# Performance work log

Hardware: AMD Instinct MI355X
Metric: run time of the kernel (lower is better)

The kernel has to match this reference:

```python
import jax, jax.numpy as jnp
import numpy as np

B, N = 2, 131072          # batch, expanded node slots (divisible by flag_size)
FEAT = 69                 # org(3) + pos(3) + uids(63)
KERNELS = 128
FLAG_SIZE = 4             # 1 << dims, dims = 2
BINS = 16                 # 1 << flag_size


def _conv1d(x, w, b, stride=1, padding='SAME'):
    # keras Conv1D: x [B,N,Cin], w [K,Cin,Cout], relu activation
    y = jax.lax.conv_general_dilated(x, w, (stride,), padding,
                                     dimension_numbers=('NWC', 'WIO', 'NWC'))
    return jax.nn.relu(y + b)


def setup_inputs() -> dict:
    key = jax.random.key(0)
    ks = jax.random.split(key, 12)

    def g(k, shape):
        fan_in = int(np.prod(shape[:-1]))
        return (jax.random.normal(k, shape, jnp.float32) / np.sqrt(fan_in)).astype(jnp.float32)

    c_x = FEAT + KERNELS                 # 197 after each pre conv concat
    c_flags = 2 * FEAT + KERNELS         # 266 flags-head input
    c_sym = c_flags + FLAG_SIZE          # 270 symbols-branch input

    return {
        'inputs': jax.random.normal(ks[0], (B, N, FEAT), jnp.float32),
        'w_pre0': g(ks[1], (3, FEAT, KERNELS)),   'b_pre0': jnp.zeros((KERNELS,), jnp.float32),
        'w_pre1': g(ks[2], (3, c_x, KERNELS)),    'b_pre1': jnp.zeros((KERNELS,), jnp.float32),
        'w_flags': g(ks[3], (c_flags, FLAG_SIZE)), 'b_flags': jnp.zeros((FLAG_SIZE,), jnp.float32),
        'w_merge': g(ks[4], (FLAG_SIZE, c_sym, KERNELS)), 'b_merge': jnp.zeros((KERNELS,), jnp.float32),
        'w_post0': g(ks[5], (3, KERNELS, KERNELS)), 'b_post0': jnp.zeros((KERNELS,), jnp.float32),
        'w_post1': g(ks[6], (3, KERNELS, KERNELS)), 'b_post1': jnp.zeros((KERNELS,), jnp.float32),
        'w_post2': g(ks[7], (3, KERNELS, KERNELS)), 'b_post2': jnp.zeros((KERNELS,), jnp.float32),
        'w_post3': g(ks[8], (3, KERNELS, KERNELS)), 'b_post3': jnp.zeros((KERNELS,), jnp.float32),
        'w_sym': g(ks[9], (KERNELS, BINS)),        'b_sym': jnp.zeros((BINS,), jnp.float32),
    }


def _forward(inputs, w_pre0, b_pre0, w_pre1, b_pre1, w_flags, b_flags,
             w_merge, b_merge, w_post0, b_post0, w_post1, b_post1,
             w_post2, b_post2, w_post3, b_post3, w_sym, b_sym):
    # pos offsets = (3, 6); pos = inputs[..., 3:5] (2 columns)
    pos = inputs[..., 3:5]
    sort = jnp.argsort(pos, axis=-2)                       # [B, N, 2]
    # gather with batch_dims=1 along node axis
    X = jnp.take_along_axis(inputs, sort[..., 1:2], axis=1)   # sorted by pos col 1
    x0 = jax.lax.stop_gradient(X)                            # [B, N, 69]
    X = jnp.concatenate([x0, _conv1d(X, w_pre0, b_pre0)], axis=-1)  # [B, N, 197]
    X = jnp.concatenate([x0, _conv1d(X, w_pre1, b_pre1)], axis=-1)  # [B, N, 197]
    X = jnp.concatenate([X, jnp.take_along_axis(inputs, sort[..., 0:1], axis=1)], axis=-1)  # [B, N, 266]

    F = jax.nn.sigmoid(X @ w_flags + b_flags)               # [B, N, 4]

    S = jax.lax.stop_gradient(jnp.concatenate([F, X], axis=-1))     # [B, N, 270]
    S = _conv1d(S, w_merge, b_merge, stride=FLAG_SIZE, padding='VALID')  # [B, N/4, 128]
    for w, b in ((w_post0, b_post0), (w_post1, b_post1), (w_post2, b_post2), (w_post3, b_post3)):
        S = _conv1d(S, w, b)
    S = jax.nn.softmax(S @ w_sym + b_sym, axis=-1)          # [B, N/4, 16]

    Fd = (F[..., 0] - F[..., 1]).reshape(F.shape[0], -1, FLAG_SIZE)  # [B, N/4, 4]
    return jnp.concatenate([Fd, S], axis=-1)                # [B, N/4, 20]


def reference(inputs, w_pre0, b_pre0, w_pre1, b_pre1, w_flags, b_flags,
              w_merge, b_merge, w_post0, b_post0, w_post1, b_post1,
              w_post2, b_post2, w_post3, b_post3, w_sym, b_sym):
    return _forward(inputs, w_pre0, b_pre0, w_pre1, b_pre1, w_flags, b_flags,
                    w_merge, b_merge, w_post0, b_post0, w_post1, b_post1,
                    w_post2, b_post2, w_post3, b_post3, w_sym, b_sym)
```

## Files before the change

### kernel.cpp

```cpp
#include <hip/hip_runtime.h>
#include <hip/hip_bf16.h>
#include <math.h>

#define NPOS 131072
#define NF   69
#define NMRG 32768
#define TILE 512
#define TPS  256
#define NSORT 4
#define EPT  8
#define CSTR 66

typedef __attribute__((ext_vector_type(8))) short short8;
typedef __bf16 bf16x8 __attribute__((ext_vector_type(8)));
typedef __attribute__((ext_vector_type(4))) float f32x4;

static __device__ inline bf16x8 as_bf16x8(short8 v){ union{short8 s; bf16x8 b;} u; u.s=v; return u.b; }
static __device__ inline short f2bf(float x){ __hip_bfloat16 h = __float2bfloat16(x); return *(short*)&h; }
static __device__ inline float bf2f(short s){ return __uint_as_float(((unsigned)(unsigned short)s)<<16); }

static __device__ inline void gld16(const short* g, short* l){
  __builtin_amdgcn_global_load_lds(
      (const __attribute__((address_space(1))) unsigned int*)g,
      (__attribute__((address_space(3))) unsigned int*)l, 16, 0, 0);
}

__global__ void k_make_keys(const float* __restrict__ inp, unsigned* __restrict__ kA,
                            unsigned* __restrict__ vA){
  unsigned t = blockIdx.x*256u + threadIdx.x;
  unsigned s = t >> 17, i = t & (NPOS-1u);
  unsigned b = s >> 1, ch = 3u + (s & 1u);
  float x = inp[((size_t)b*NPOS + i)*NF + ch];
  unsigned u = __float_as_uint(x);
  u = (u & 0x80000000u) ? ~u : (u | 0x80000000u);
  kA[t] = u; vA[t] = i;
}

__global__ __launch_bounds__(256) void k_hist(const unsigned* __restrict__ src,
                                              unsigned* __restrict__ hist, int shift){
  __shared__ unsigned h[256];
  int tid = threadIdx.x;
  h[tid] = 0u; __syncthreads();
  int s = blockIdx.x >> 8, tile = blockIdx.x & 255;
  const unsigned* ks = src + (size_t)s*NPOS + (size_t)tile*TILE;
  #pragma unroll
  for (int r = 0; r < TILE/256; ++r){
    unsigned d = (ks[r*256 + tid] >> shift) & 255u;
    atomicAdd(&h[d], 1u);
  }
  __syncthreads();
  hist[s*65536 + tid*TPS + tile] = h[tid];
}

__global__ __launch_bounds__(256) void k_scan(unsigned* __restrict__ hist){
  __shared__ unsigned tot[256];
  int tid = threadIdx.x; int s = blockIdx.x;
  unsigned* g = hist + s*65536;
  unsigned sum = 0;
  for (int q = 0; q < TPS; ++q) sum += g[tid*TPS + q];
  tot[tid] = sum;
  __syncthreads();
  if (tid == 0){
    unsigned run = 0;
    for (int t = 0; t < 256; ++t){ unsigned tmp = tot[t]; tot[t] = run; run += tmp; }
  }
  __syncthreads();
  unsigned run = tot[tid];
  for (int q = 0; q < TPS; ++q){ unsigned tmp = g[tid*TPS+q]; g[tid*TPS+q] = run; run += tmp; }
}

__global__ __launch_bounds__(64) void k_scatter(const unsigned* __restrict__ srcK,
    const unsigned* __restrict__ srcV, unsigned* __restrict__ dstK, unsigned* __restrict__ dstV,
    const unsigned* __restrict__ off, int shift){
  __shared__ unsigned short cnt[256*CSTR];
  int tid = threadIdx.x;
  short8* cz = (short8*)cnt;
  short8 z = {0,0,0,0,0,0,0,0};
  for (int idx = tid; idx < 256*CSTR/8; idx += 64) cz[idx] = z;
  __syncthreads();
  int s = blockIdx.x >> 8, tile = blockIdx.x & 255;
  const unsigned* ks = srcK + (size_t)s*NPOS + (size_t)tile*TILE;
  const unsigned* vs = srcV + (size_t)s*NPOS + (size_t)tile*TILE;
  unsigned k8[EPT], v8[EPT];
  #pragma unroll
  for (int r = 0; r < EPT; ++r){
    k8[r] = ks[tid*EPT + r];
    v8[r] = vs[tid*EPT + r];
    unsigned d = (k8[r] >> shift) & 255u;
    cnt[d*CSTR + tid]++;
  }
  __syncthreads();
  #pragma unroll
  for (int dd = 0; dd < 4; ++dd){
    int d = tid + dd*64;
    unsigned run = 0;
    for (int t = 0; t < 64; ++t){ unsigned tmp = cnt[d*CSTR + t]; cnt[d*CSTR + t] = (unsigned short)run; run += tmp; }
  }
  __syncthreads();
  const unsigned* ob = off + s*65536;
  #pragma unroll
  for (int r = 0; r < EPT; ++r){
    unsigned d = (k8[r] >> shift) & 255u;
    unsigned rk = cnt[d*CSTR + tid];
    cnt[d*CSTR + tid] = (unsigned short)(rk + 1u);
    unsigned pos = ob[d*TPS + tile] + rk;
    dstK[(size_t)s*NPOS + pos] = k8[r];
    dstV[(size_t)s*NPOS + pos] = v8[r];
  }
}

__global__ __launch_bounds__(256) void k_gath(const float* __restrict__ inp,
    const unsigned* __restrict__ P1, const unsigned* __restrict__ P0,
    short* __restrict__ XA, short* __restrict__ Xcat, int b){
  int t = blockIdx.x*256 + threadIdx.x;
  int i = t >> 7, c = t & 127;
  if (c < 69){
    short s1 = f2bf(inp[((size_t)b*NPOS + P1[i])*NF + c]);
    XA[(size_t)i*224 + 128 + c] = s1;
    Xcat[(size_t)i*272 + 132 + c] = s1;
    Xcat[(size_t)i*272 + 201 + c] = f2bf(inp[((size_t)b*NPOS + P0[i])*NF + c]);
  } else if (c == 69){
    Xcat[(size_t)i*272 + 270] = 0;
    Xcat[(size_t)i*272 + 271] = 0;
  }
}

__global__ void k_prepB(const float* __restrict__ w, short* __restrict__ out,
                        int KC, int NQ, int mode, int total){
  int t = blockIdx.x*256 + threadIdx.x;
  if (t >= total) return;
  int lane = t & 63, ni = (t>>6) & 1, ksub = (t>>7) & 1;
  int rest = t >> 8;
  int q = rest % NQ;
  int wv = rest / NQ;
  int tap = q / KC, cc = q - tap*KC;
  int nn = wv*32 + ni*16 + (lane & 15);
  int chb = cc*64 + ksub*32 + ((lane >> 4) & 3)*8;
  short o[8];
  #pragma unroll
  for (int e = 0; e < 8; ++e){
    int ch = chb + e;
    float val = 0.f;
    if (mode == 0){ if (ch < 69)  val = w[((size_t)tap*69  + ch)*128 + nn]; }
    else if (mode == 1){
      if (ch < 128)      val = w[((size_t)tap*197 + 69 + ch)*128 + nn];
      else if (ch < 197) val = w[((size_t)tap*197 + ch - 128)*128 + nn];
    }
    else if (mode == 2){ if (ch < 128) val = w[((size_t)tap*128 + ch)*128 + nn]; }
    else {
      int tm = ch / 272, cm = ch - tm*272;
      int orig = -1;
      if (cm < 128)      orig = 73 + cm;
      else if (cm < 201) orig = cm - 128;
      else if (cm < 270) orig = cm;
      if (orig >= 0) val = w[((size_t)tm*270 + orig)*128 + nn];
    }
    o[e] = f2bf(val);
  }
  *(short8*)(out + (size_t)t*8) = *(short8*)o;
}

__global__ void k_prepWf(const float* __restrict__ wf, float* __restrict__ out){
  int t = blockIdx.x*256 + threadIdx.x;
  if (t >= 1088) return;
  int c = t >> 2, q = t & 3;
  float v = 0.f;
  if (c < 128)                 v = wf[(69 + c)*4 + q];
  else if (c >= 132 && c < 201) v = wf[(c - 132)*4 + q];
  else if (c >= 201 && c < 270) v = wf[(197 + c - 201)*4 + q];
  out[t] = v;
}

#define OSTR 132

template<int CPAD>
__global__ __launch_bounds__(256) void k_conv3p(
    const short* __restrict__ src, int sstride, int coff, int cin,
    const short* __restrict__ wB, const float* __restrict__ bias,
    short* __restrict__ dst, int dstride, int n)
{
  constexpr int KC = CPAD/64;
  constexpr int NSTEP2 = 3*KC*2;
  constexpr int PF = 4;
  constexpr int ASTR = CPAD + 8;
  constexpr int AG = CPAD/8;
  constexpr size_t ABYTES = (size_t)66*ASTR*2;
  constexpr size_t OBYTES = (size_t)64*OSTR*4;
  constexpr size_t LBYTES = (ABYTES > OBYTES) ? ABYTES : OBYTES;
  __shared__ __attribute__((aligned(16))) char LDS[LBYTES];
  short* A_s = (short*)LDS;
  float* OT  = (float*)LDS;
  int tid = threadIdx.x;
  int i0 = blockIdx.x*64;
  int wv = tid >> 6, lane = tid & 63;
  int lm = lane & 15, lk = lane >> 4;

  const short* wBw = wB + (size_t)wv*NSTEP2*1024 + (size_t)lane*8;
  auto LB = [&](int ss, int ni){
    return as_bf16x8(*(const short8*)(wBw + (ss*2 + ni)*512));
  };
  bf16x8 bq[PF][2];
  #pragma unroll
  for (int s = 0; s < PF; ++s){ bq[s][0] = LB(s,0); bq[s][1] = LB(s,1); }

  for (int idx = tid; idx < 66*AG; idx += 256){
    int r = idx / AG, g = idx - r*AG;
    int pos = i0 - 1 + r;
    short8 v = {0,0,0,0,0,0,0,0};
    if (pos >= 0 && pos < n && g*8 < cin){
      const short* sp = src + (size_t)pos*sstride + coff + g*8;
      if (g*8 + 8 <= cin) v = *(const short8*)sp;
      else { for (int j = 0; g*8 + j < cin; ++j) v[j] = sp[j]; }
    }
    *(short8*)(A_s + r*ASTR + g*8) = v;
  }
  __syncthreads();

  f32x4 acc[4][2] = {};
  #pragma unroll
  for (int ss = 0; ss < NSTEP2; ++ss){
    int slot = ss % PF;
    bf16x8 b0 = bq[slot][0], b1 = bq[slot][1];
    if (ss + PF < NSTEP2){ bq[slot][0] = LB(ss+PF,0); bq[slot][1] = LB(ss+PF,1); }
    int q = ss >> 1, ksub = ss & 1;
    int tp = q / KC, c = q - tp*KC;
    bf16x8 a[4];
    #pragma unroll
    for (int mi = 0; mi < 4; ++mi)
      a[mi] = as_bf16x8(*(const short8*)(A_s + (mi*16+lm+tp)*ASTR + c*64 + ksub*32 + lk*8));
    #pragma unroll
    for (int mi = 0; mi < 4; ++mi){
      acc[mi][0] = __builtin_amdgcn_mfma_f32_16x16x32_bf16(a[mi], b0, acc[mi][0], 0, 0, 0);
      acc[mi][1] = __builtin_amdgcn_mfma_f32_16x16x32_bf16(a[mi], b1, acc[mi][1], 0, 0, 0);
    }
  }
  __syncthreads();
  float b0s = bias[wv*32 + lm], b1s = bias[wv*32 + 16 + lm];
  #pragma unroll
  for (int mi = 0; mi < 4; ++mi)
    #pragma unroll
    for (int ni = 0; ni < 2; ++ni){
      float bb = ni ? b1s : b0s;
      #pragma unroll
      for (int r = 0; r < 4; ++r)
        OT[(mi*16 + lk*4 + r)*OSTR + wv*32 + ni*16 + lm] = fmaxf(acc[mi][ni][r] + bb, 0.f);
    }
  __syncthreads();
  {
    int r = tid >> 2, q = tid & 3;
    const float* row = OT + r*OSTR + q*32;
    short o[32];
    #pragma unroll
    for (int jc = 0; jc < 8; ++jc){
      f32x4 v = *(const f32x4*)(row + jc*4);
      #pragma unroll
      for (int e = 0; e < 4; ++e) o[jc*4+e] = f2bf(v[e]);
    }
    short* dp = dst + (size_t)(i0 + r)*dstride + q*32;
    #pragma unroll
    for (int v8 = 0; v8 < 4; ++v8) *(short8*)(dp + v8*8) = *(short8*)(o + v8*8);
  }
}

__global__ __launch_bounds__(256) void k_mergem3(const short* __restrict__ Xf,
    const short* __restrict__ wB, const float* __restrict__ bias, short* __restrict__ dst)
{
  constexpr size_t OBYTES = (size_t)64*OSTR*4;
  __shared__ __attribute__((aligned(16))) char LDS[OBYTES];
  short* A_s = (short*)LDS;
  float* OT  = (float*)LDS;
  int tid = threadIdx.x;
  int j0 = blockIdx.x*64;
  int wv = tid >> 6, lane = tid & 63;
  int lm = lane & 15, lk = lane >> 4;
  auto stageA = [&](int s){
    #pragma unroll
    for (int it = 0; it < 2; ++it){
      int slot = it*256 + tid;
      int r = slot >> 3, kv = slot & 7;
      const short* gp = Xf + (size_t)(j0 + r)*1088 + s*64 + ((kv ^ (r&7))*8);
      gld16(gp, A_s + (s&1)*4096 + slot*8);
    }
  };
  const short* wBl = wB + (size_t)wv*17*2048 + (size_t)lane*8;
  auto LB = [&](int s, int ks, int ni){
    return as_bf16x8(*(const short8*)(wBl + ((size_t)(s*2 + ks)*2 + ni)*512));
  };
  bf16x8 c00 = LB(0,0,0), c01 = LB(0,0,1), c10 = LB(0,1,0), c11 = LB(0,1,1);
  stageA(0);
  __syncthreads();
  f32x4 acc[4][2] = {};
  for (int s = 0; s < 17; ++s){
    bf16x8 n00, n01, n10, n11;
    if (s < 16){
      n00 = LB(s+1,0,0); n01 = LB(s+1,0,1); n10 = LB(s+1,1,0); n11 = LB(s+1,1,1);
      stageA(s+1);
    }
    const short* Ab = A_s + (s&1)*4096;
    bf16x8 a[4];
    #pragma unroll
    for (int mi = 0; mi < 4; ++mi){
      int r = mi*16 + lm;
      a[mi] = as_bf16x8(*(const short8*)(Ab + r*64 + ((lk ^ (r&7))*8)));
    }
    #pragma unroll
    for (int mi = 0; mi < 4; ++mi){
      acc[mi][0] = __builtin_amdgcn_mfma_f32_16x16x32_bf16(a[mi], c00, acc[mi][0], 0, 0, 0);
      acc[mi][1] = __builtin_amdgcn_mfma_f32_16x16x32_bf16(a[mi], c01, acc[mi][1], 0, 0, 0);
    }
    #pragma unroll
    for (int mi = 0; mi < 4; ++mi){
      int r = mi*16 + lm;
      a[mi] = as_bf16x8(*(const short8*)(Ab + r*64 + (((4+lk) ^ (r&7))*8)));
    }
    #pragma unroll
    for (int mi = 0; mi < 4; ++mi){
      acc[mi][0] = __builtin_amdgcn_mfma_f32_16x16x32_bf16(a[mi], c10, acc[mi][0], 0, 0, 0);
      acc[mi][1] = __builtin_amdgcn_mfma_f32_16x16x32_bf16(a[mi], c11, acc[mi][1], 0, 0, 0);
    }
    __syncthreads();
    c00 = n00; c01 = n01; c10 = n10; c11 = n11;
  }
  float b0 = bias[wv*32 + lm], b1 = bias[wv*32 + 16 + lm];
  #pragma unroll
  for (int mi = 0; mi < 4; ++mi)
    #pragma unroll
    for (int ni = 0; ni < 2; ++ni){
      float bb = ni ? b1 : b0;
      #pragma unroll
      for (int r = 0; r < 4; ++r)
        OT[(mi*16 + lk*4 + r)*OSTR + wv*32 + ni*16 + lm] = fmaxf(acc[mi][ni][r] + bb, 0.f);
    }
  __syncthreads();
  {
    int r = tid >> 2, q = tid & 3;
    const float* row = OT + r*OSTR + q*32;
    short o[32];
    #pragma unroll
    for (int jc = 0; jc < 8; ++jc){
      f32x4 v = *(const f32x4*)(row + jc*4);
      #pragma unroll
      for (int e = 0; e < 4; ++e) o[jc*4+e] = f2bf(v[e]);
    }
    short* dp = dst + (size_t)(j0 + r)*128 + q*32;
    #pragma unroll
    for (int v8 = 0; v8 < 4; ++v8) *(short8*)(dp + v8*8) = *(short8*)(o + v8*8);
  }
}

__global__ __launch_bounds__(256) void k_flags2(short* __restrict__ Xcat,
    const float* __restrict__ Wf2, const float* __restrict__ bf, float* __restrict__ F){
  size_t i = (size_t)blockIdx.x*256 + threadIdx.x;
  const short* x = Xcat + i*272;
  float a0 = bf[0], a1 = bf[1], a2 = bf[2], a3 = bf[3];
  for (int g = 0; g < 34; ++g){
    short8 x8 = *(const short8*)(x + g*8);
    #pragma unroll
    for (int e = 0; e < 8; ++e){
      float xv = bf2f(x8[e]);
      const float* w = Wf2 + (g*8+e)*4;
      a0 = fmaf(xv,w[0],a0); a1 = fmaf(xv,w[1],a1); a2 = fmaf(xv,w[2],a2); a3 = fmaf(xv,w[3],a3);
    }
  }
  float f0 = 1.f/(1.f+expf(-a0)), f1 = 1.f/(1.f+expf(-a1));
  float f2 = 1.f/(1.f+expf(-a2)), f3 = 1.f/(1.f+expf(-a3));
  float* f = F + i*4;
  f[0]=f0; f[1]=f1; f[2]=f2; f[3]=f3;
  short* xc = Xcat + i*272 + 128;
  xc[0]=f2bf(f0); xc[1]=f2bf(f1); xc[2]=f2bf(f2); xc[3]=f2bf(f3);
}

__global__ __launch_bounds__(256) void k_out(const short* __restrict__ S,
    const float* __restrict__ F, const float* __restrict__ Ws, const float* __restrict__ bs,
    float* __restrict__ out, int b){
  size_t j = (size_t)blockIdx.x*256 + threadIdx.x;
  float l[16];
  #pragma unroll
  for (int t = 0; t < 16; ++t) l[t] = bs[t];
  const short* s = S + j*128;
  for (int g = 0; g < 16; ++g){
    short8 x8 = *(const short8*)(s + g*8);
    #pragma unroll
    for (int e = 0; e < 8; ++e){
      float x = bf2f(x8[e]);
      const float* w = Ws + (g*8+e)*16;
      #pragma unroll
      for (int t = 0; t < 16; ++t) l[t] = fmaf(x, w[t], l[t]);
    }
  }
  float m = l[0];
  #pragma unroll
  for (int t = 1; t < 16; ++t) m = fmaxf(m, l[t]);
  float sum = 0.f;
  #pragma unroll
  for (int t = 0; t < 16; ++t){ l[t] = expf(l[t]-m); sum += l[t]; }
  float inv = 1.f/sum;
  float* o = out + ((size_t)b*NMRG + j)*20;
  #pragma unroll
  for (int k = 0; k < 4; ++k){
    size_t r = (size_t)(4*j + k)*4;
    o[k] = F[r] - F[r+1];
  }
  #pragma unroll
  for (int t = 0; t < 16; ++t) o[4+t] = l[t]*inv;
}

extern "C" void kernel_launch(void* const* d_in, const int* in_sizes, int n_in,
                              void* d_out, int out_size, void* d_ws, size_t ws_size,
                              hipStream_t stream){
  const float* inp     = (const float*)d_in[0];
  const float* w_pre0  = (const float*)d_in[1];
  const float* b_pre0  = (const float*)d_in[2];
  const float* w_pre1  = (const float*)d_in[3];
  const float* b_pre1  = (const float*)d_in[4];
  const float* w_flags = (const float*)d_in[5];
  const float* b_flags = (const float*)d_in[6];
  const float* w_merge = (const float*)d_in[7];
  const float* b_merge = (const float*)d_in[8];
  const float* w_post[4] = {(const float*)d_in[9], (const float*)d_in[11],
                            (const float*)d_in[13], (const float*)d_in[15]};
  const float* b_post[4] = {(const float*)d_in[10], (const float*)d_in[12],
                            (const float*)d_in[14], (const float*)d_in[16]};
  const float* w_sym   = (const float*)d_in[17];
  const float* b_sym   = (const float*)d_in[18];
  float* outp = (float*)d_out;

  char* p = (char*)d_ws;
  unsigned* kA = (unsigned*)p; p += (size_t)NSORT*NPOS*4;
  unsigned* vA = (unsigned*)p; p += (size_t)NSORT*NPOS*4;
  unsigned* kB = (unsigned*)p; p += (size_t)NSORT*NPOS*4;
  unsigned* vB = (unsigned*)p; p += (size_t)NSORT*NPOS*4;
  unsigned* hist = (unsigned*)p; p += (size_t)NSORT*65536*4;
  short* XA   = (short*)p; p += (size_t)NPOS*224*2;
  short* Xcat = (short*)p; p += (size_t)NPOS*272*2;
  float* Fbuf = (float*)p; p += (size_t)NPOS*4*4;
  short* M0   = (short*)p; p += (size_t)NMRG*128*2;
  short* M1   = (short*)p; p += (size_t)NMRG*128*2;
  short* wb0  = (short*)p; p += (size_t)3*2*8192*2;
  short* wb1  = (short*)p; p += (size_t)3*4*8192*2;
  short* wbq0 = (short*)p; p += (size_t)3*2*8192*2;
  short* wbq1 = (short*)p; p += (size_t)3*2*8192*2;
  short* wbq2 = (short*)p; p += (size_t)3*2*8192*2;
  short* wbq3 = (short*)p; p += (size_t)3*2*8192*2;
  short* wbm  = (short*)p; p += (size_t)17*8192*2;
  float* wf2  = (float*)p; p += (size_t)272*4*4;
  if ((size_t)(p - (char*)d_ws) > ws_size) return;
  short* wbq[4] = {wbq0, wbq1, wbq2, wbq3};

  k_prepB<<<(6144 +255)/256, 256, 0, stream>>>(w_pre0, wb0, 2, 6, 0, 6144);
  k_prepB<<<(12288+255)/256, 256, 0, stream>>>(w_pre1, wb1, 4, 12, 1, 12288);
  for (int i = 0; i < 4; ++i)
    k_prepB<<<(6144+255)/256, 256, 0, stream>>>(w_post[i], wbq[i], 2, 6, 2, 6144);
  k_prepB<<<(17408+255)/256, 256, 0, stream>>>(w_merge, wbm, 17, 17, 3, 17408);
  k_prepWf<<<5, 256, 0, stream>>>(w_flags, wf2);

  k_make_keys<<<NSORT*NPOS/256, 256, 0, stream>>>(inp, kA, vA);
  unsigned *sk = kA, *sv = vA, *dk = kB, *dv = vB;
  for (int pass = 0; pass < 4; ++pass){
    int shift = pass*8;
    k_hist<<<NSORT*TPS, 256, 0, stream>>>(sk, hist, shift);
    k_scan<<<NSORT, 256, 0, stream>>>(hist);
    k_scatter<<<NSORT*TPS, 64, 0, stream>>>(sk, sv, dk, dv, hist, shift);
    unsigned* t;
    t = sk; sk = dk; dk = t;
    t = sv; sv = dv; dv = t;
  }
  for (int b = 0; b < 2; ++b){
    const unsigned* P0 = sv + (size_t)(b*2+0)*NPOS;
    const unsigned* P1 = sv + (size_t)(b*2+1)*NPOS;
    k_gath<<<NPOS*128/256, 256, 0, stream>>>(inp, P1, P0, XA, Xcat, b);
    k_conv3p<128><<<NPOS/64, 256, 0, stream>>>(XA, 224, 128, 69,  wb0, b_pre0, XA,   224, NPOS);
    k_conv3p<256><<<NPOS/64, 256, 0, stream>>>(XA, 224, 0,   197, wb1, b_pre1, Xcat, 272, NPOS);
    k_flags2<<<NPOS/256, 256, 0, stream>>>(Xcat, wf2, b_flags, Fbuf);
    k_mergem3<<<NMRG/64, 256, 0, stream>>>(Xcat, wbm, b_merge, M0);
    k_conv3p<128><<<NMRG/64, 256, 0, stream>>>(M0, 128, 0, 128, wbq[0], b_post[0], M1, 128, NMRG);
    k_conv3p<128><<<NMRG/64, 256, 0, stream>>>(M1, 128, 0, 128, wbq[1], b_post[1], M0, 128, NMRG);
    k_conv3p<128><<<NMRG/64, 256, 0, stream>>>(M0, 128, 0, 128, wbq[2], b_post[2], M1, 128, NMRG);
    k_conv3p<128><<<NMRG/64, 256, 0, stream>>>(M1, 128, 0, 128, wbq[3], b_post[3], M0, 128, NMRG);
    k_out<<<NMRG/256, 256, 0, stream>>>(M0, Fbuf, w_sym, b_sym, outp, b);
  }
}
```

Before: 640.3 us.

## Enlarge radix sort tiles and vectorize gather via pre-converted bf16 input

Radix sort tiles grow from 512 to 2048 keys with 128-thread scatter blocks, so there are fewer histogram entries and blocks per pass. The row gather now runs on a padded bf16 copy of the input (72 columns), so each thread moves 16-byte vectors instead of scalar strided floats. The Xcat row stride is widened to 288 so the second copy of the raw features starts 16-byte aligned, and the merge weights, flag weights and merge step count are remapped to match. This adds a conversion pass and a larger LDS counter array in scatter, which may lower occupancy, and the merge GEMM does slightly more work.

```diff
diff --git a/kernel.cpp b/kernel.cpp
--- a/kernel.cpp
+++ b/kernel.cpp
@@ -5,13 +5,14 @@
 #define NPOS 131072
 #define NF   69
 #define NMRG 32768
-#define TILE 512
-#define TPS  256
+#define TILE 2048
+#define TPS  64
 #define NSORT 4
-#define EPT  8
-#define CSTR 66
+#define EPT  16
+#define XCW  288
 
 typedef __attribute__((ext_vector_type(8))) short short8;
+typedef __attribute__((ext_vector_type(4))) short s16x4;
 typedef __bf16 bf16x8 __attribute__((ext_vector_type(8)));
 typedef __attribute__((ext_vector_type(4))) float f32x4;
 
@@ -41,21 +42,20 @@
   __shared__ unsigned h[256];
   int tid = threadIdx.x;
   h[tid] = 0u; __syncthreads();
-  int s = blockIdx.x >> 8, tile = blockIdx.x & 255;
+  int s = blockIdx.x / TPS, tile = blockIdx.x % TPS;
   const unsigned* ks = src + (size_t)s*NPOS + (size_t)tile*TILE;
-  #pragma unroll
   for (int r = 0; r < TILE/256; ++r){
     unsigned d = (ks[r*256 + tid] >> shift) & 255u;
     atomicAdd(&h[d], 1u);
   }
   __syncthreads();
-  hist[s*65536 + tid*TPS + tile] = h[tid];
+  hist[s*16384 + tid*TPS + tile] = h[tid];
 }
 
 __global__ __launch_bounds__(256) void k_scan(unsigned* __restrict__ hist){
   __shared__ unsigned tot[256];
   int tid = threadIdx.x; int s = blockIdx.x;
-  unsigned* g = hist + s*65536;
+  unsigned* g = hist + s*16384;
   unsigned sum = 0;
   for (int q = 0; q < TPS; ++q) sum += g[tid*TPS + q];
   tot[tid] = sum;
@@ -69,16 +69,15 @@
   for (int q = 0; q < TPS; ++q){ unsigned tmp = g[tid*TPS+q]; g[tid*TPS+q] = run; run += tmp; }
 }
 
-__global__ __launch_bounds__(64) void k_scatter(const unsigned* __restrict__ srcK,
+__global__ __launch_bounds__(128) void k_scatter(const unsigned* __restrict__ srcK,
     const unsigned* __restrict__ srcV, unsigned* __restrict__ dstK, unsigned* __restrict__ dstV,
     const unsigned* __restrict__ off, int shift){
-  __shared__ unsigned short cnt[256*CSTR];
+  __shared__ unsigned short cnt[256*128];
   int tid = threadIdx.x;
-  short8* cz = (short8*)cnt;
-  short8 z = {0,0,0,0,0,0,0,0};
-  for (int idx = tid; idx < 256*CSTR/8; idx += 64) cz[idx] = z;
-  __syncthreads();
-  int s = blockIdx.x >> 8, tile = blockIdx.x & 255;
+  unsigned* cz = (unsigned*)cnt;
+  for (int idx = tid; idx < 256*128/2; idx += 128) cz[idx] = 0u;
+  __syncthreads();
+  int s = blockIdx.x / TPS, tile = blockIdx.x % TPS;
   const unsigned* ks = srcK + (size_t)s*NPOS + (size_t)tile*TILE;
   const unsigned* vs = srcV + (size_t)s*NPOS + (size_t)tile*TILE;
   unsigned k8[EPT], v8[EPT];
@@ -87,41 +86,62 @@
     k8[r] = ks[tid*EPT + r];
     v8[r] = vs[tid*EPT + r];
     unsigned d = (k8[r] >> shift) & 255u;
-    cnt[d*CSTR + tid]++;
-  }
-  __syncthreads();
-  #pragma unroll
-  for (int dd = 0; dd < 4; ++dd){
-    int d = tid + dd*64;
+    cnt[d*128 + tid]++;
+  }
+  __syncthreads();
+  for (int dd = 0; dd < 2; ++dd){
+    int d = tid + dd*128;
     unsigned run = 0;
-    for (int t = 0; t < 64; ++t){ unsigned tmp = cnt[d*CSTR + t]; cnt[d*CSTR + t] = (unsigned short)run; run += tmp; }
-  }
-  __syncthreads();
-  const unsigned* ob = off + s*65536;
+    for (int t = 0; t < 128; ++t){ unsigned tmp = cnt[d*128 + t]; cnt[d*128 + t] = (unsigned short)run; run += tmp; }
+  }
+  __syncthreads();
+  const unsigned* ob = off + s*16384;
   #pragma unroll
   for (int r = 0; r < EPT; ++r){
     unsigned d = (k8[r] >> shift) & 255u;
-    unsigned rk = cnt[d*CSTR + tid];
-    cnt[d*CSTR + tid] = (unsigned short)(rk + 1u);
+    unsigned rk = cnt[d*128 + tid];
+    cnt[d*128 + tid] = (unsigned short)(rk + 1u);
     unsigned pos = ob[d*TPS + tile] + rk;
     dstK[(size_t)s*NPOS + pos] = k8[r];
     dstV[(size_t)s*NPOS + pos] = v8[r];
   }
 }
 
-__global__ __launch_bounds__(256) void k_gath(const float* __restrict__ inp,
+__global__ __launch_bounds__(256) void k_cvt(const float* __restrict__ inp,
+                                             short* __restrict__ inpb, int b){
+  int t = blockIdx.x*256 + threadIdx.x;
+  int i = t/9, q = t - i*9;
+  const float* sp = inp + ((size_t)b*NPOS + i)*NF + q*8;
+  short o[8];
+  #pragma unroll
+  for (int e = 0; e < 8; ++e){
+    int c = q*8 + e;
+    o[e] = (c < NF) ? f2bf(sp[e]) : (short)0;
+  }
+  *(short8*)(inpb + (size_t)i*72 + q*8) = *(short8*)o;
+}
+
+__global__ __launch_bounds__(256) void k_gath2(const short* __restrict__ inpb,
     const unsigned* __restrict__ P1, const unsigned* __restrict__ P0,
-    short* __restrict__ XA, short* __restrict__ Xcat, int b){
+    short* __restrict__ XA, short* __restrict__ Xcat){
   int t = blockIdx.x*256 + threadIdx.x;
-  int i = t >> 7, c = t & 127;
-  if (c < 69){
-    short s1 = f2bf(inp[((size_t)b*NPOS + P1[i])*NF + c]);
-    XA[(size_t)i*224 + 128 + c] = s1;
-    Xcat[(size_t)i*272 + 132 + c] = s1;
-    Xcat[(size_t)i*272 + 201 + c] = f2bf(inp[((size_t)b*NPOS + P0[i])*NF + c]);
-  } else if (c == 69){
-    Xcat[(size_t)i*272 + 270] = 0;
-    Xcat[(size_t)i*272 + 271] = 0;
+  int i = t/18, u = t - i*18;
+  int p = u/9, q = u - p*9;
+  if (p){
+    short8 v = *(const short8*)(inpb + (size_t)P1[i]*72 + q*8);
+    *(short8*)(XA + (size_t)i*224 + 128 + q*8) = v;
+    s16x4 lo = {v[0],v[1],v[2],v[3]}, hi = {v[4],v[5],v[6],v[7]};
+    *(s16x4*)(Xcat + (size_t)i*XCW + 132 + q*8) = lo;
+    *(s16x4*)(Xcat + (size_t)i*XCW + 136 + q*8) = hi;
+  } else {
+    short8 v = *(const short8*)(inpb + (size_t)P0[i]*72 + q*8);
+    *(short8*)(Xcat + (size_t)i*XCW + 208 + q*8) = v;
+    if (q == 8){
+      s16x4 z4 = {0,0,0,0};
+      *(s16x4*)(Xcat + (size_t)i*XCW + 204) = z4;
+      short8 z8 = {0,0,0,0,0,0,0,0};
+      *(short8*)(Xcat + (size_t)i*XCW + 280) = z8;
+    }
   }
 }
 
@@ -148,11 +168,11 @@
     }
     else if (mode == 2){ if (ch < 128) val = w[((size_t)tap*128 + ch)*128 + nn]; }
     else {
-      int tm = ch / 272, cm = ch - tm*272;
+      int tm = ch / XCW, cm = ch - tm*XCW;
       int orig = -1;
-      if (cm < 128)      orig = 73 + cm;
-      else if (cm < 201) orig = cm - 128;
-      else if (cm < 270) orig = cm;
+      if (cm < 128)                     orig = 73 + cm;
+      else if (cm < 201)                orig = cm - 128;
+      else if (cm >= 208 && cm < 277)   orig = cm - 7;
       if (orig >= 0) val = w[((size_t)tm*270 + orig)*128 + nn];
     }
     o[e] = f2bf(val);
@@ -162,12 +182,12 @@
 
 __global__ void k_prepWf(const float* __restrict__ wf, float* __restrict__ out){
   int t = blockIdx.x*256 + threadIdx.x;
-  if (t >= 1088) return;
+  if (t >= XCW*4) return;
   int c = t >> 2, q = t & 3;
   float v = 0.f;
-  if (c < 128)                 v = wf[(69 + c)*4 + q];
+  if (c < 128)                  v = wf[(69 + c)*4 + q];
   else if (c >= 132 && c < 201) v = wf[(c - 132)*4 + q];
-  else if (c >= 201 && c < 270) v = wf[(197 + c - 201)*4 + q];
+  else if (c >= 208 && c < 277) v = wf[(197 + c - 208)*4 + q];
   out[t] = v;
 }
 
@@ -265,6 +285,7 @@
 __global__ __launch_bounds__(256) void k_mergem3(const short* __restrict__ Xf,
     const short* __restrict__ wB, const float* __restrict__ bias, short* __restrict__ dst)
 {
+  constexpr int NS = 4*XCW/64;
   constexpr size_t OBYTES = (size_t)64*OSTR*4;
   __shared__ __attribute__((aligned(16))) char LDS[OBYTES];
   short* A_s = (short*)LDS;
@@ -278,11 +299,11 @@
     for (int it = 0; it < 2; ++it){
       int slot = it*256 + tid;
       int r = slot >> 3, kv = slot & 7;
-      const short* gp = Xf + (size_t)(j0 + r)*1088 + s*64 + ((kv ^ (r&7))*8);
+      const short* gp = Xf + (size_t)(j0 + r)*(4*XCW) + s*64 + ((kv ^ (r&7))*8);
       gld16(gp, A_s + (s&1)*4096 + slot*8);
     }
   };
-  const short* wBl = wB + (size_t)wv*17*2048 + (size_t)lane*8;
+  const short* wBl = wB + (size_t)wv*NS*2048 + (size_t)lane*8;
   auto LB = [&](int s, int ks, int ni){
     return as_bf16x8(*(const short8*)(wBl + ((size_t)(s*2 + ks)*2 + ni)*512));
   };
@@ -290,9 +311,9 @@
   stageA(0);
   __syncthreads();
   f32x4 acc[4][2] = {};
-  for (int s = 0; s < 17; ++s){
+  for (int s = 0; s < NS; ++s){
     bf16x8 n00, n01, n10, n11;
-    if (s < 16){
+    if (s < NS-1){
       n00 = LB(s+1,0,0); n01 = LB(s+1,0,1); n10 = LB(s+1,1,0); n11 = LB(s+1,1,1);
       stageA(s+1);
     }
@@ -351,9 +372,9 @@
 __global__ __launch_bounds__(256) void k_flags2(short* __restrict__ Xcat,
     const float* __restrict__ Wf2, const float* __restrict__ bf, float* __restrict__ F){
   size_t i = (size_t)blockIdx.x*256 + threadIdx.x;
-  const short* x = Xcat + i*272;
+  const short* x = Xcat + i*XCW;
   float a0 = bf[0], a1 = bf[1], a2 = bf[2], a3 = bf[3];
-  for (int g = 0; g < 34; ++g){
+  for (int g = 0; g < XCW/8; ++g){
     short8 x8 = *(const short8*)(x + g*8);
     #pragma unroll
     for (int e = 0; e < 8; ++e){
@@ -366,7 +387,7 @@
   float f2 = 1.f/(1.f+expf(-a2)), f3 = 1.f/(1.f+expf(-a3));
   float* f = F + i*4;
   f[0]=f0; f[1]=f1; f[2]=f2; f[3]=f3;
-  short* xc = Xcat + i*272 + 128;
+  short* xc = Xcat + i*XCW + 128;
   xc[0]=f2bf(f0); xc[1]=f2bf(f1); xc[2]=f2bf(f2); xc[3]=f2bf(f3);
 }
 
@@ -430,9 +451,10 @@
   unsigned* vA = (unsigned*)p; p += (size_t)NSORT*NPOS*4;
   unsigned* kB = (unsigned*)p; p += (size_t)NSORT*NPOS*4;
   unsigned* vB = (unsigned*)p; p += (size_t)NSORT*NPOS*4;
-  unsigned* hist = (unsigned*)p; p += (size_t)NSORT*65536*4;
+  unsigned* hist = (unsigned*)p; p += (size_t)NSORT*16384*4;
+  short* inpb = (short*)p; p += (size_t)NPOS*72*2;
   short* XA   = (short*)p; p += (size_t)NPOS*224*2;
-  short* Xcat = (short*)p; p += (size_t)NPOS*272*2;
+  short* Xcat = (short*)p; p += (size_t)NPOS*XCW*2;
   float* Fbuf = (float*)p; p += (size_t)NPOS*4*4;
   short* M0   = (short*)p; p += (size_t)NMRG*128*2;
   short* M1   = (short*)p; p += (size_t)NMRG*128*2;
@@ -442,8 +464,8 @@
   short* wbq1 = (short*)p; p += (size_t)3*2*8192*2;
   short* wbq2 = (short*)p; p += (size_t)3*2*8192*2;
   short* wbq3 = (short*)p; p += (size_t)3*2*8192*2;
-  short* wbm  = (short*)p; p += (size_t)17*8192*2;
-  float* wf2  = (float*)p; p += (size_t)272*4*4;
+  short* wbm  = (short*)p; p += (size_t)18*8192*2;
+  float* wf2  = (float*)p; p += (size_t)XCW*4*4;
   if ((size_t)(p - (char*)d_ws) > ws_size) return;
   short* wbq[4] = {wbq0, wbq1, wbq2, wbq3};
 
@@ -451,8 +473,8 @@
   k_prepB<<<(12288+255)/256, 256, 0, stream>>>(w_pre1, wb1, 4, 12, 1, 12288);
   for (int i = 0; i < 4; ++i)
     k_prepB<<<(6144+255)/256, 256, 0, stream>>>(w_post[i], wbq[i], 2, 6, 2, 6144);
-  k_prepB<<<(17408+255)/256, 256, 0, stream>>>(w_merge, wbm, 17, 17, 3, 17408);
-  k_prepWf<<<5, 256, 0, stream>>>(w_flags, wf2);
+  k_prepB<<<(18432+255)/256, 256, 0, stream>>>(w_merge, wbm, 18, 18, 3, 18432);
+  k_prepWf<<<(XCW*4+255)/256, 256, 0, stream>>>(w_flags, wf2);
 
   k_make_keys<<<NSORT*NPOS/256, 256, 0, stream>>>(inp, kA, vA);
   unsigned *sk = kA, *sv = vA, *dk = kB, *dv = vB;
@@ -460,7 +482,7 @@
     int shift = pass*8;
     k_hist<<<NSORT*TPS, 256, 0, stream>>>(sk, hist, shift);
     k_scan<<<NSORT, 256, 0, stream>>>(hist);
-    k_scatter<<<NSORT*TPS, 64, 0, stream>>>(sk, sv, dk, dv, hist, shift);
+    k_scatter<<<NSORT*TPS, 128, 0, stream>>>(sk, sv, dk, dv, hist, shift);
     unsigned* t;
     t = sk; sk = dk; dk = t;
     t = sv; sv = dv; dv = t;
@@ -468,9 +490,10 @@
   for (int b = 0; b < 2; ++b){
     const unsigned* P0 = sv + (size_t)(b*2+0)*NPOS;
     const unsigned* P1 = sv + (size_t)(b*2+1)*NPOS;
-    k_gath<<<NPOS*128/256, 256, 0, stream>>>(inp, P1, P0, XA, Xcat, b);
+    k_cvt<<<NPOS*9/256, 256, 0, stream>>>(inp, inpb, b);
+    k_gath2<<<NPOS*18/256, 256, 0, stream>>>(inpb, P1, P0, XA, Xcat);
     k_conv3p<128><<<NPOS/64, 256, 0, stream>>>(XA, 224, 128, 69,  wb0, b_pre0, XA,   224, NPOS);
-    k_conv3p<256><<<NPOS/64, 256, 0, stream>>>(XA, 224, 0,   197, wb1, b_pre1, Xcat, 272, NPOS);
+    k_conv3p<256><<<NPOS/64, 256, 0, stream>>>(XA, 224, 0,   197, wb1, b_pre1, Xcat, XCW, NPOS);
     k_flags2<<<NPOS/256, 256, 0, stream>>>(Xcat, wf2, b_flags, Fbuf);
     k_mergem3<<<NMRG/64, 256, 0, stream>>>(Xcat, wbm, b_merge, M0);
     k_conv3p<128><<<NMRG/64, 256, 0, stream>>>(M0, 128, 0, 128, wbq[0], b_post[0], M1, 128, NMRG);
```

New measurement: 598.8 us. -6.5%, faster.
